# Optimization experiments

Hardware: AMD Instinct MI355X
Metric: run time of the kernel (lower is better)

The kernel has to match this reference:

```python
import jax, jax.numpy as jnp
import numpy as np

B, N, D, H = 4, 1024, 1024, 16
NP = N - 1  # prototypes; +1 CLS slot -> n_valid == N
HD = D // H
LN_EPS = 1e-5


def _build_spatial_sim(key):
    centers = jax.random.uniform(key, (NP, 2), dtype=jnp.float32) * 10.0
    diff = centers[:, None, :] - centers[None, :, :]
    d2 = jnp.sum(diff * diff, axis=-1)           # squared pairwise distance
    dist = jnp.sqrt(d2)
    sigma = dist.mean()                           # spatial_sigma = mean cdist
    sim = jnp.exp(-d2 / (2.0 * sigma * sigma))
    sim = sim / sim.max()
    ext = jnp.zeros((NP + 1, NP + 1), dtype=jnp.float32)
    ext = ext.at[0, :].set(1.0).at[:, 0].set(1.0).at[1:, 1:].set(sim)
    return ext


def setup_inputs() -> dict:
    key = jax.random.key(0)
    kc, kx, kq, kp = jax.random.split(key, 4)
    spatial_sim = _build_spatial_sim(kc)          # [N, N] buffer
    x = jax.random.normal(kx, (B, N, D), dtype=jnp.float32)
    gamma = jnp.ones((D,), dtype=jnp.float32)
    beta = jnp.zeros((D,), dtype=jnp.float32)
    w_qkv = jax.random.normal(kq, (D, 3 * D), dtype=jnp.float32) * 0.02
    w_proj = jax.random.normal(kp, (D, D), dtype=jnp.float32) * 0.02
    b_proj = jnp.zeros((D,), dtype=jnp.float32)
    swl = jnp.float32(np.log(0.3 / 0.7))          # inverse_sigmoid(0.3)
    return {"x": x, "gamma": gamma, "beta": beta, "w_qkv": w_qkv,
            "w_proj": w_proj, "b_proj": b_proj,
            "spatial_weight_logit": swl, "spatial_sim": spatial_sim}


def reference(x, gamma, beta, w_qkv, w_proj, b_proj, spatial_weight_logit, spatial_sim):
    b, n, d = x.shape
    scale = HD ** (-0.5)
    # LayerNorm (biased variance, eps=1e-5)
    mu = x.mean(axis=-1, keepdims=True)
    var = jnp.mean((x - mu) ** 2, axis=-1, keepdims=True)
    x_norm = (x - mu) / jnp.sqrt(var + LN_EPS) * gamma + beta
    # QKV projection -> [B, H, N, HD] each
    qkv = (x_norm @ w_qkv).reshape(b, n, 3, H, HD)
    qkv = jnp.transpose(qkv, (2, 0, 3, 1, 4))
    q, k, v = qkv[0], qkv[1], qkv[2]
    scores = jnp.einsum('bhnd,bhmd->bhnm', q, k) * scale
    alpha = jax.nn.sigmoid(spatial_weight_logit)
    # blend feature attention with fixed spatial similarity, then softmax
    attn = jax.nn.softmax((1.0 - alpha) * scores + alpha * spatial_sim[None, None], axis=-1)
    out = jnp.einsum('bhnm,bhmd->bhnd', attn, v)
    out = jnp.transpose(out, (0, 2, 1, 3)).reshape(b, n, d)
    out = out @ w_proj + b_proj
    return x + out
```

## Files before the change

### kernel.cpp

```cpp
#include <hip/hip_runtime.h>

#define Bz 4
#define Nn 1024
#define Dd 1024
#define Hh 16
#define HD 64
#define SCALE 0.125f
#define LN_EPS 1e-5f

typedef __attribute__((ext_vector_type(8))) __bf16 bf16x8;
typedef __attribute__((ext_vector_type(4))) float f32x4;

static __device__ inline unsigned short f2bf(float f) {
    unsigned int u = __float_as_uint(f);
    u += 0x7fffu + ((u >> 16) & 1u);
    return (unsigned short)(u >> 16);
}

static __device__ inline bf16x8 ldfrag(const unsigned short* p) {
    return *(const bf16x8*)p;
}

static __device__ __forceinline__ void glds16(const unsigned short* g, unsigned short* l) {
    __builtin_amdgcn_global_load_lds((const __attribute__((address_space(1))) void*)g,
                                     (__attribute__((address_space(3))) void*)l, 16, 0, 0);
}

__global__ __launch_bounds__(256) void prep_kernel(const float* __restrict__ x,
                                                   const float* __restrict__ gamma,
                                                   const float* __restrict__ beta,
                                                   unsigned short* __restrict__ xn,
                                                   const float* __restrict__ w_qkv,
                                                   unsigned short* __restrict__ wqkvT,
                                                   const float* __restrict__ w_proj,
                                                   unsigned short* __restrict__ wprojT) {
    __shared__ float tile[32][33];
    int blk = blockIdx.x;
    int tid = threadIdx.x;

    if (blk < 4096) {
        const float* xr = x + (size_t)blk * Dd;
        float4 v = ((const float4*)xr)[tid];
        float s = v.x + v.y + v.z + v.w;
        float ss = v.x * v.x + v.y * v.y + v.z * v.z + v.w * v.w;
        for (int o = 32; o > 0; o >>= 1) {
            s += __shfl_down(s, o);
            ss += __shfl_down(ss, o);
        }
        float* red = &tile[0][0];
        int wid = tid >> 6;
        if ((tid & 63) == 0) { red[wid * 2] = s; red[wid * 2 + 1] = ss; }
        __syncthreads();
        float tot = red[0] + red[2] + red[4] + red[6];
        float tot2 = red[1] + red[3] + red[5] + red[7];
        float mu = tot * (1.0f / Dd);
        float var = tot2 * (1.0f / Dd) - mu * mu;
        float inv = rsqrtf(var + LN_EPS);
        float4 g = ((const float4*)gamma)[tid];
        float4 b = ((const float4*)beta)[tid];
        ushort4 o4;
        o4.x = f2bf((v.x - mu) * inv * g.x + b.x);
        o4.y = f2bf((v.y - mu) * inv * g.y + b.y);
        o4.z = f2bf((v.z - mu) * inv * g.z + b.z);
        o4.w = f2bf((v.w - mu) * inv * g.w + b.w);
        ((ushort4*)(xn + (size_t)blk * Dd))[tid] = o4;
    } else {
        const float* in;
        unsigned short* out;
        int cols, c0, r0;
        if (blk < 7168) {
            int idx = blk - 4096;
            in = w_qkv; out = wqkvT; cols = 3072;
            c0 = (idx % 96) * 32; r0 = (idx / 96) * 32;
        } else {
            int idx = blk - 7168;
            in = w_proj; out = wprojT; cols = 1024;
            c0 = (idx % 32) * 32; r0 = (idx / 32) * 32;
        }
        int tx = tid & 31, ty = tid >> 5;
        #pragma unroll
        for (int i = 0; i < 32; i += 8)
            tile[ty + i][tx] = in[(size_t)(r0 + ty + i) * cols + c0 + tx];
        __syncthreads();
        #pragma unroll
        for (int i = 0; i < 32; i += 8)
            out[(size_t)(c0 + ty + i) * 1024 + r0 + tx] = f2bf(tile[tx][ty + i]);
    }
}


__global__ __launch_bounds__(256) void gemm_qkv(const unsigned short* __restrict__ A,
                                                const unsigned short* __restrict__ Bt,
                                                unsigned short* __restrict__ qb,
                                                unsigned short* __restrict__ kb,
                                                unsigned short* __restrict__ vtb) {
    __shared__ unsigned short sA[8192], sB[8192];
    int tid = threadIdx.x;
    int w = tid >> 6, lane = tid & 63, lrow = lane & 15, quad = lane >> 4;
    int wm = w >> 1, wn = w & 1;
    int rowbase = blockIdx.y * 128;
    int colbase = blockIdx.x * 128;

    int srow = tid >> 3;
    int gch = ((tid & 7) - (srow >> 1)) & 7;
    const unsigned short* gA = A + (size_t)(rowbase + srow) * 1024 + gch * 8;
    const unsigned short* gB = Bt + (size_t)(colbase + srow) * 1024 + gch * 8;
    unsigned short* lA = sA + w * 512;
    unsigned short* lB = sB + w * 512;

    int bs0 = ((quad + (lrow >> 1)) & 7) * 8;
    int bs1 = ((4 + quad + (lrow >> 1)) & 7) * 8;
    const unsigned short* fa = sA + (wm * 64 + lrow) * 64;
    const unsigned short* fb = sB + (wn * 64 + lrow) * 64;

    f32x4 acc[4][4];
    #pragma unroll
    for (int i = 0; i < 4; i++)
        #pragma unroll
        for (int j = 0; j < 4; j++)
            acc[i][j] = (f32x4){0.f, 0.f, 0.f, 0.f};

    for (int k0 = 0; k0 < 1024; k0 += 64) {
        __syncthreads();
        #pragma unroll
        for (int c = 0; c < 4; c++) {
            glds16(gA + (size_t)c * 32768 + k0, lA + c * 2048);
            glds16(gB + (size_t)c * 32768 + k0, lB + c * 2048);
        }
        __syncthreads();
        #pragma unroll
        for (int s = 0; s < 2; s++) {
            int bo = s ? bs1 : bs0;
            bf16x8 a[4], b[4];
            #pragma unroll
            for (int i = 0; i < 4; i++) a[i] = *(const bf16x8*)(fa + i * 1024 + bo);
            #pragma unroll
            for (int j = 0; j < 4; j++) b[j] = *(const bf16x8*)(fb + j * 1024 + bo);
            #pragma unroll
            for (int i = 0; i < 4; i++)
                #pragma unroll
                for (int j = 0; j < 4; j++)
                    acc[i][j] = __builtin_amdgcn_mfma_f32_16x16x32_bf16(a[i], b[j], acc[i][j], 0, 0, 0);
        }
    }

    if (colbase < 2048) {
        #pragma unroll
        for (int j = 0; j < 4; j++) {
            int col = colbase + wn * 64 + j * 16 + lrow;
            int s = col >> 10, rem = col & 1023;
            int h = rem >> 6, e = rem & 63;
            unsigned short* dst = (s == 0) ? qb : kb;
            #pragma unroll
            for (int i = 0; i < 4; i++) {
                #pragma unroll
                for (int r = 0; r < 4; r++) {
                    int R = rowbase + wm * 64 + i * 16 + quad * 4 + r;
                    int bb = R >> 10, n = R & 1023;
                    dst[(((size_t)(bb * Hh + h)) * Nn + n) * HD + e] = f2bf(acc[i][j][r]);
                }
            }
        }
    } else {
        int bb = rowbase >> 10;
        int nbase = (rowbase & 1023) + wm * 64;
        unsigned short* sc = sA + w * 2048;
        int er = lane >> 2, nc = lane & 3;
        #pragma unroll
        for (int j = 0; j < 4; j++) {
            __syncthreads();
            int ebase = colbase + wn * 64 + j * 16 - 2048;
            int h = ebase >> 6, e0 = ebase & 63;
            #pragma unroll
            for (int i = 0; i < 4; i++) {
                uint2 pk;
                pk.x = (unsigned)f2bf(acc[i][j][0]) | ((unsigned)f2bf(acc[i][j][1]) << 16);
                pk.y = (unsigned)f2bf(acc[i][j][2]) | ((unsigned)f2bf(acc[i][j][3]) << 16);
                *(uint2*)(sc + lrow * 68 + i * 16 + quad * 4) = pk;
            }
            __syncthreads();
            unsigned short* vrow = vtb + ((size_t)((bb * Hh + h) * HD) + e0 + er) * Nn + nbase;
            #pragma unroll
            for (int c = 0; c < 4; c++) {
                uint2 v = *(const uint2*)(sc + er * 68 + c * 16 + nc * 4);
                *(uint2*)(vrow + c * 16 + nc * 4) = v;
            }
        }
    }
}

__global__ __launch_bounds__(256) void gemm_proj(const unsigned short* __restrict__ A,
                                                 const unsigned short* __restrict__ Bt,
                                                 const float* __restrict__ bias,
                                                 const float* __restrict__ x,
                                                 float* __restrict__ out) {
    __shared__ unsigned short sA[8192], sB[8192];
    int tid = threadIdx.x;
    int w = tid >> 6, lane = tid & 63, lrow = lane & 15, quad = lane >> 4;
    int wm = w >> 1, wn = w & 1;
    int rowbase = blockIdx.y * 128;
    int colbase = blockIdx.x * 128;

    int srow = tid >> 3;
    int gch = ((tid & 7) - (srow >> 1)) & 7;
    const unsigned short* gA = A + (size_t)(rowbase + srow) * 1024 + gch * 8;
    const unsigned short* gB = Bt + (size_t)(colbase + srow) * 1024 + gch * 8;
    unsigned short* lA = sA + w * 512;
    unsigned short* lB = sB + w * 512;

    int bs0 = ((quad + (lrow >> 1)) & 7) * 8;
    int bs1 = ((4 + quad + (lrow >> 1)) & 7) * 8;
    const unsigned short* fa = sA + (wm * 64 + lrow) * 64;
    const unsigned short* fb = sB + (wn * 64 + lrow) * 64;

    f32x4 acc[4][4];
    #pragma unroll
    for (int i = 0; i < 4; i++)
        #pragma unroll
        for (int j = 0; j < 4; j++)
            acc[i][j] = (f32x4){0.f, 0.f, 0.f, 0.f};

    for (int k0 = 0; k0 < 1024; k0 += 64) {
        __syncthreads();
        #pragma unroll
        for (int c = 0; c < 4; c++) {
            glds16(gA + (size_t)c * 32768 + k0, lA + c * 2048);
            glds16(gB + (size_t)c * 32768 + k0, lB + c * 2048);
        }
        __syncthreads();
        #pragma unroll
        for (int s = 0; s < 2; s++) {
            int bo = s ? bs1 : bs0;
            bf16x8 a[4], b[4];
            #pragma unroll
            for (int i = 0; i < 4; i++) a[i] = *(const bf16x8*)(fa + i * 1024 + bo);
            #pragma unroll
            for (int j = 0; j < 4; j++) b[j] = *(const bf16x8*)(fb + j * 1024 + bo);
            #pragma unroll
            for (int i = 0; i < 4; i++)
                #pragma unroll
                for (int j = 0; j < 4; j++)
                    acc[i][j] = __builtin_amdgcn_mfma_f32_16x16x32_bf16(a[i], b[j], acc[i][j], 0, 0, 0);
        }
    }

    #pragma unroll
    for (int j = 0; j < 4; j++) {
        int col = colbase + wn * 64 + j * 16 + lrow;
        float bc = bias[col];
        #pragma unroll
        for (int i = 0; i < 4; i++) {
            #pragma unroll
            for (int r = 0; r < 4; r++) {
                int R = rowbase + wm * 64 + i * 16 + quad * 4 + r;
                out[(size_t)R * 1024 + col] = acc[i][j][r] + bc + x[(size_t)R * 1024 + col];
            }
        }
    }
}

#define LOG2E 1.4426950408889634f
__global__ __launch_bounds__(256, 2) void attn_kernel(const unsigned short* __restrict__ qb,
                                                      const unsigned short* __restrict__ kb,
                                                      const unsigned short* __restrict__ vtb,
                                                      const float* __restrict__ sim,
                                                      const float* __restrict__ swl,
                                                      unsigned short* __restrict__ aout) {
    int h = blockIdx.y, bb = blockIdx.z;
    int n0 = blockIdx.x * 128;
    int tid = threadIdx.x;
    int w = tid >> 6, lane = tid & 63;
    int lrow = lane & 15, quad = lane >> 4;
    const unsigned short* q = qb + ((size_t)(bb * Hh + h)) * Nn * HD;
    const unsigned short* k = kb + ((size_t)(bb * Hh + h)) * Nn * HD;
    const unsigned short* vt = vtb + ((size_t)(bb * Hh + h)) * HD * Nn;
    float alpha = 1.f / (1.f + __expf(-swl[0]));
    float c1 = (1.f - alpha) * SCALE * LOG2E;
    float a2 = alpha * LOG2E;

    __shared__ unsigned short sK[2][4096];
    __shared__ unsigned short sV[2][4096];
    __shared__ unsigned short sP[8192];

    int qr0 = n0 + w * 32;
    bf16x8 qf[2][2];
    #pragma unroll
    for (int g = 0; g < 2; g++) {
        qf[g][0] = ldfrag(q + (size_t)(qr0 + g * 16 + lrow) * HD + quad * 8);
        qf[g][1] = ldfrag(q + (size_t)(qr0 + g * 16 + lrow) * HD + 32 + quad * 8);
    }

    f32x4 o[2][4];
    #pragma unroll
    for (int g = 0; g < 2; g++)
        #pragma unroll
        for (int et = 0; et < 4; et++) o[g][et] = (f32x4){0.f, 0.f, 0.f, 0.f};
    float rsum[2] = {0.f, 0.f};

    int bs0 = (quad + (lrow >> 1)) & 7;
    int bs1 = (4 + quad + (lrow >> 1)) & 7;
    unsigned short* sPw = sP + (w * 32) * 64;

    const float* gS0 = sim + (size_t)(qr0 + lrow) * Nn + quad * 4;
    const float* gS1 = gS0 + (size_t)16 * Nn;

    #pragma unroll
    for (int i = 0; i < 2; i++) {
        int slot = i * 256 + tid;
        int row = slot >> 3;
        int cg = ((slot & 7) - (row >> 1)) & 7;
        glds16(k + (size_t)row * HD + cg * 8, &sK[0][0] + i * 2048 + w * 512);
        glds16(vt + (size_t)row * Nn + cg * 8, &sV[0][0] + i * 2048 + w * 512);
    }
    float4 sm[4][2];
    #pragma unroll
    for (int ks = 0; ks < 4; ks++) {
        sm[ks][0] = *(const float4*)(gS0 + ks * 16);
        sm[ks][1] = *(const float4*)(gS1 + ks * 16);
    }
    __syncthreads();

    for (int t = 0; t < 16; t++) {
        int cur = t & 1;
        float4 smN[4][2];
        if (t < 15) {
            int m1 = (t + 1) * 64;
            #pragma unroll
            for (int i = 0; i < 2; i++) {
                int slot = i * 256 + tid;
                int row = slot >> 3;
                int cg = ((slot & 7) - (row >> 1)) & 7;
                glds16(k + (size_t)(m1 + row) * HD + cg * 8, &sK[cur ^ 1][0] + i * 2048 + w * 512);
                glds16(vt + (size_t)row * Nn + m1 + cg * 8, &sV[cur ^ 1][0] + i * 2048 + w * 512);
            }
            #pragma unroll
            for (int ks = 0; ks < 4; ks++) {
                smN[ks][0] = *(const float4*)(gS0 + m1 + ks * 16);
                smN[ks][1] = *(const float4*)(gS1 + m1 + ks * 16);
            }
        }

        const unsigned short* sKc = sK[cur];
        const unsigned short* sVc = sV[cur];
        #pragma unroll
        for (int ks = 0; ks < 4; ks++) {
            const unsigned short* kr = sKc + (ks * 16 + lrow) * 64;
            bf16x8 ak0 = *(const bf16x8*)(kr + bs0 * 8);
            bf16x8 ak1 = *(const bf16x8*)(kr + bs1 * 8);
            #pragma unroll
            for (int g = 0; g < 2; g++) {
                f32x4 c = (f32x4){0.f, 0.f, 0.f, 0.f};
                c = __builtin_amdgcn_mfma_f32_16x16x32_bf16(ak0, qf[g][0], c, 0, 0, 0);
                c = __builtin_amdgcn_mfma_f32_16x16x32_bf16(ak1, qf[g][1], c, 0, 0, 0);
                float e0 = __builtin_amdgcn_exp2f(c1 * c[0] + a2 * sm[ks][g].x);
                float e1 = __builtin_amdgcn_exp2f(c1 * c[1] + a2 * sm[ks][g].y);
                float e2 = __builtin_amdgcn_exp2f(c1 * c[2] + a2 * sm[ks][g].z);
                float e3 = __builtin_amdgcn_exp2f(c1 * c[3] + a2 * sm[ks][g].w);
                rsum[g] += (e0 + e1) + (e2 + e3);
                uint2 pk;
                pk.x = (__float_as_uint(e0) >> 16) | (__float_as_uint(e1) & 0xffff0000u);
                pk.y = (__float_as_uint(e2) >> 16) | (__float_as_uint(e3) & 0xffff0000u);
                int row = g * 16 + lrow;
                int chv = (ks * 2 + (quad >> 1)) ^ (row & 7);
                *(uint2*)(sPw + row * 64 + chv * 8 + (quad & 1) * 4) = pk;
            }
        }

        __builtin_amdgcn_s_setprio(1);
        #pragma unroll
        for (int ms = 0; ms < 2; ms++) {
            bf16x8 pa[2];
            #pragma unroll
            for (int g = 0; g < 2; g++) {
                int row = g * 16 + lrow;
                int chp = (ms * 4 + quad) ^ (row & 7);
                pa[g] = *(const bf16x8*)(sPw + row * 64 + chp * 8);
            }
            #pragma unroll
            for (int et = 0; et < 4; et++) {
                int e = et * 16 + lrow;
                int slot = (ms * 4 + quad + (e >> 1)) & 7;
                bf16x8 vb = *(const bf16x8*)(sVc + e * 64 + slot * 8);
                #pragma unroll
                for (int g = 0; g < 2; g++)
                    o[g][et] = __builtin_amdgcn_mfma_f32_16x16x32_bf16(pa[g], vb, o[g][et], 0, 0, 0);
            }
        }
        __builtin_amdgcn_s_setprio(0);

        __syncthreads();
        if (t < 15) {
            #pragma unroll
            for (int ks = 0; ks < 4; ks++) {
                sm[ks][0] = smN[ks][0];
                sm[ks][1] = smN[ks][1];
            }
        }
    }

    #pragma unroll
    for (int g = 0; g < 2; g++) {
        rsum[g] += __shfl_xor(rsum[g], 16);
        rsum[g] += __shfl_xor(rsum[g], 32);
    }

    #pragma unroll
    for (int g = 0; g < 2; g++)
        #pragma unroll
        for (int r = 0; r < 4; r++) {
            float inv = 1.f / __shfl(rsum[g], quad * 4 + r);
            int qn = qr0 + g * 16 + quad * 4 + r;
            #pragma unroll
            for (int et = 0; et < 4; et++)
                aout[((size_t)bb * Nn + qn) * Dd + h * HD + et * 16 + lrow]
                    = f2bf(o[g][et][r] * inv);
        }
}

extern "C" void kernel_launch(void* const* d_in, const int* in_sizes, int n_in,
                              void* d_out, int out_size, void* d_ws, size_t ws_size,
                              hipStream_t stream) {
    const float* x      = (const float*)d_in[0];
    const float* gamma  = (const float*)d_in[1];
    const float* beta   = (const float*)d_in[2];
    const float* w_qkv  = (const float*)d_in[3];
    const float* w_proj = (const float*)d_in[4];
    const float* b_proj = (const float*)d_in[5];
    const float* swl    = (const float*)d_in[6];
    const float* sim    = (const float*)d_in[7];
    float* out = (float*)d_out;

    unsigned short* ws = (unsigned short*)d_ws;
    unsigned short* xn     = ws;
    unsigned short* wqkvT  = xn + 4194304;
    unsigned short* wprojT = wqkvT + 3145728;
    unsigned short* qb     = wprojT + 1048576;
    unsigned short* kb     = qb + 4194304;
    unsigned short* vtb    = kb + 4194304;
    unsigned short* aout   = vtb + 4194304;

    prep_kernel<<<8192, 256, 0, stream>>>(x, gamma, beta, xn, w_qkv, wqkvT, w_proj, wprojT);
    gemm_qkv<<<dim3(24, 32), 256, 0, stream>>>(xn, wqkvT, qb, kb, vtb);
    attn_kernel<<<dim3(8, 16, 4), 256, 0, stream>>>(qb, kb, vtb, sim, swl, aout);
    gemm_proj<<<dim3(8, 32), 256, 0, stream>>>(aout, wprojT, b_proj, x, out);
}
```

Measured before the change: 202.0 us.

## Keep softmax probabilities in registers by permuting K rows to match MFMA layout

Removes the shared-memory staging buffer for the bf16 probability tile. K rows are loaded into LDS in a permuted order, and the spatial-similarity offsets are remapped to match, so the QK^T MFMA output fragments already sit in the A-operand layout the PV MFMA expects. Each lane can then build the PV operand by bit-casting its packed registers. This drops the LDS store/load round trip and the LDS footprint, at the cost of extra live registers and a more intricate index mapping that must stay consistent between K rows and sim columns.

```diff
diff --git a/kernel.cpp b/kernel.cpp
--- a/kernel.cpp
+++ b/kernel.cpp
@@ -10,6 +10,7 @@
 
 typedef __attribute__((ext_vector_type(8))) __bf16 bf16x8;
 typedef __attribute__((ext_vector_type(4))) float f32x4;
+typedef __attribute__((ext_vector_type(4))) unsigned int uint4v;
 
 static __device__ inline unsigned short f2bf(float f) {
     unsigned int u = __float_as_uint(f);
@@ -280,7 +281,6 @@
 
     __shared__ unsigned short sK[2][4096];
     __shared__ unsigned short sV[2][4096];
-    __shared__ unsigned short sP[8192];
 
     int qr0 = n0 + w * 32;
     bf16x8 qf[2][2];
@@ -299,24 +299,26 @@
 
     int bs0 = (quad + (lrow >> 1)) & 7;
     int bs1 = (4 + quad + (lrow >> 1)) & 7;
-    unsigned short* sPw = sP + (w * 32) * 64;
-
-    const float* gS0 = sim + (size_t)(qr0 + lrow) * Nn + quad * 4;
+
+    const float* gS0 = sim + (size_t)(qr0 + lrow) * Nn + quad * 8;
     const float* gS1 = gS0 + (size_t)16 * Nn;
 
-    #pragma unroll
-    for (int i = 0; i < 2; i++) {
-        int slot = i * 256 + tid;
-        int row = slot >> 3;
-        int cg = ((slot & 7) - (row >> 1)) & 7;
-        glds16(k + (size_t)row * HD + cg * 8, &sK[0][0] + i * 2048 + w * 512);
-        glds16(vt + (size_t)row * Nn + cg * 8, &sV[0][0] + i * 2048 + w * 512);
-    }
+    int rowA = tid >> 3, rowB = (256 + tid) >> 3;
+    int cgA = ((tid & 7) - (rowA >> 1)) & 7;
+    int cgB = ((tid & 7) - (rowB >> 1)) & 7;
+    int growA = ((rowA & 28) << 1) | ((rowA & 32) >> 3) | (rowA & 3);
+    int growB = ((rowB & 28) << 1) | ((rowB & 32) >> 3) | (rowB & 3);
+
+    glds16(k + (size_t)growA * HD + cgA * 8, &sK[0][0] + w * 512);
+    glds16(k + (size_t)growB * HD + cgB * 8, &sK[0][0] + 2048 + w * 512);
+    glds16(vt + (size_t)rowA * Nn + cgA * 8, &sV[0][0] + w * 512);
+    glds16(vt + (size_t)rowB * Nn + cgB * 8, &sV[0][0] + 2048 + w * 512);
     float4 sm[4][2];
     #pragma unroll
     for (int ks = 0; ks < 4; ks++) {
-        sm[ks][0] = *(const float4*)(gS0 + ks * 16);
-        sm[ks][1] = *(const float4*)(gS1 + ks * 16);
+        int koff = ((ks & 1) << 5) | ((ks >> 1) << 2);
+        sm[ks][0] = *(const float4*)(gS0 + koff);
+        sm[ks][1] = *(const float4*)(gS1 + koff);
     }
     __syncthreads();
 
@@ -325,23 +327,23 @@
         float4 smN[4][2];
         if (t < 15) {
             int m1 = (t + 1) * 64;
-            #pragma unroll
-            for (int i = 0; i < 2; i++) {
-                int slot = i * 256 + tid;
-                int row = slot >> 3;
-                int cg = ((slot & 7) - (row >> 1)) & 7;
-                glds16(k + (size_t)(m1 + row) * HD + cg * 8, &sK[cur ^ 1][0] + i * 2048 + w * 512);
-                glds16(vt + (size_t)row * Nn + m1 + cg * 8, &sV[cur ^ 1][0] + i * 2048 + w * 512);
-            }
+            unsigned short* dK = &sK[cur ^ 1][0];
+            unsigned short* dV = &sV[cur ^ 1][0];
+            glds16(k + (size_t)(m1 + growA) * HD + cgA * 8, dK + w * 512);
+            glds16(k + (size_t)(m1 + growB) * HD + cgB * 8, dK + 2048 + w * 512);
+            glds16(vt + (size_t)rowA * Nn + m1 + cgA * 8, dV + w * 512);
+            glds16(vt + (size_t)rowB * Nn + m1 + cgB * 8, dV + 2048 + w * 512);
             #pragma unroll
             for (int ks = 0; ks < 4; ks++) {
-                smN[ks][0] = *(const float4*)(gS0 + m1 + ks * 16);
-                smN[ks][1] = *(const float4*)(gS1 + m1 + ks * 16);
+                int koff = ((ks & 1) << 5) | ((ks >> 1) << 2);
+                smN[ks][0] = *(const float4*)(gS0 + m1 + koff);
+                smN[ks][1] = *(const float4*)(gS1 + m1 + koff);
             }
         }
 
         const unsigned short* sKc = sK[cur];
         const unsigned short* sVc = sV[cur];
+        uint2 pk[2][4];
         #pragma unroll
         for (int ks = 0; ks < 4; ks++) {
             const unsigned short* kr = sKc + (ks * 16 + lrow) * 64;
@@ -357,12 +359,8 @@
                 float e2 = __builtin_amdgcn_exp2f(c1 * c[2] + a2 * sm[ks][g].z);
                 float e3 = __builtin_amdgcn_exp2f(c1 * c[3] + a2 * sm[ks][g].w);
                 rsum[g] += (e0 + e1) + (e2 + e3);
-                uint2 pk;
-                pk.x = (__float_as_uint(e0) >> 16) | (__float_as_uint(e1) & 0xffff0000u);
-                pk.y = (__float_as_uint(e2) >> 16) | (__float_as_uint(e3) & 0xffff0000u);
-                int row = g * 16 + lrow;
-                int chv = (ks * 2 + (quad >> 1)) ^ (row & 7);
-                *(uint2*)(sPw + row * 64 + chv * 8 + (quad & 1) * 4) = pk;
+                pk[g][ks].x = (__float_as_uint(e0) >> 16) | (__float_as_uint(e1) & 0xffff0000u);
+                pk[g][ks].y = (__float_as_uint(e2) >> 16) | (__float_as_uint(e3) & 0xffff0000u);
             }
         }
 
@@ -372,9 +370,10 @@
             bf16x8 pa[2];
             #pragma unroll
             for (int g = 0; g < 2; g++) {
-                int row = g * 16 + lrow;
-                int chp = (ms * 4 + quad) ^ (row & 7);
-                pa[g] = *(const bf16x8*)(sPw + row * 64 + chp * 8);
+                uint4v u;
+                u.x = pk[g][ms].x;  u.y = pk[g][ms].y;
+                u.z = pk[g][ms + 2].x;  u.w = pk[g][ms + 2].y;
+                pa[g] = __builtin_bit_cast(bf16x8, u);
             }
             #pragma unroll
             for (int et = 0; et < 4; et++) {
```

After: 194.1 us. 3.9% less time.
